# Kernel optimization log

Measured on AMD Instinct MI355X. Metric: run time of the kernel, lower is better.

Reference implementation:

```python
import jax, jax.numpy as jnp
import numpy as np

N_PROD, N_CUST = 100000, 50000
HID, OUT = 128, 64
E_PP, E_PC, E_LB = 800000, 800000, 400000


def sage(x_src, x_dst, src, dst, Wl, bl, Wr, n_dst):
    # PyG SAGEConv (mean aggr): lin_l(mean_{j->i} x_j) + lin_r(x_i); bias on lin_l only
    msg = x_src[src]                                             # [E, d] gather
    s = jax.ops.segment_sum(msg, dst, num_segments=n_dst)        # [n_dst, d]
    cnt = jax.ops.segment_sum(jnp.ones((src.shape[0],), x_src.dtype), dst, num_segments=n_dst)
    mean = s / jnp.maximum(cnt, 1.0)[:, None]
    return mean @ Wl.T + bl + x_dst @ Wr.T


def setup_inputs() -> dict:
    key = jax.random.key(0)
    ks = iter(jax.random.split(key, 40))

    def lin_w(i, o):
        return (jax.random.normal(next(ks), (o, i), jnp.float32) / np.sqrt(i))

    inp = {}
    inp['x_product'] = jax.random.normal(next(ks), (N_PROD, HID), jnp.float32)
    inp['x_customer'] = jax.random.normal(next(ks), (N_CUST, HID), jnp.float32)
    inp['ei_pp'] = jax.random.randint(next(ks), (2, E_PP), 0, N_PROD)
    src_pc = jax.random.randint(next(ks), (1, E_PC), 0, N_PROD)
    dst_pc = jax.random.randint(next(ks), (1, E_PC), 0, N_CUST)
    inp['ei_pc'] = jnp.concatenate([src_pc, dst_pc], axis=0)
    row = jax.random.randint(next(ks), (1, E_LB), 0, N_CUST)
    col = jax.random.randint(next(ks), (1, E_LB), 0, N_PROD)
    inp['edge_label_index'] = jnp.concatenate([row, col], axis=0)

    # ItemGNNEncoder params
    inp['it_W1l'], inp['it_W1r'] = lin_w(HID, HID), lin_w(HID, HID)
    inp['it_b1'] = jnp.zeros((HID,), jnp.float32)
    inp['it_W2l'], inp['it_W2r'] = lin_w(HID, HID), lin_w(HID, HID)
    inp['it_b2'] = jnp.zeros((HID,), jnp.float32)
    inp['it_Wlin'] = lin_w(HID, OUT)
    inp['it_blin'] = jnp.zeros((OUT,), jnp.float32)
    # UserGNNEncoder params
    inp['us_W1l'], inp['us_W1r'] = lin_w(HID, HID), lin_w(HID, HID)
    inp['us_b1'] = jnp.zeros((HID,), jnp.float32)
    inp['us_W2l'], inp['us_W2r'] = lin_w(HID, HID), lin_w(HID, HID)
    inp['us_b2'] = jnp.zeros((HID,), jnp.float32)
    inp['us_W3l'], inp['us_W3r'] = lin_w(HID, HID), lin_w(HID, HID)
    inp['us_b3'] = jnp.zeros((HID,), jnp.float32)
    inp['us_Wlin'] = lin_w(HID, OUT)
    inp['us_blin'] = jnp.zeros((OUT,), jnp.float32)
    # EdgeDecoder params
    inp['de_W1'] = lin_w(2 * OUT, OUT)
    inp['de_b1'] = jnp.zeros((OUT,), jnp.float32)
    inp['de_W2'] = lin_w(OUT, 1)
    inp['de_b2'] = jnp.zeros((1,), jnp.float32)
    return inp


def reference(x_product, x_customer, ei_pp, ei_pc, edge_label_index,
              it_W1l, it_b1, it_W1r, it_W2l, it_b2, it_W2r, it_Wlin, it_blin,
              us_W1l, us_b1, us_W1r, us_W2l, us_b2, us_W2r, us_W3l, us_b3, us_W3r,
              us_Wlin, us_blin, de_W1, de_b1, de_W2, de_b2):
    pp_s, pp_d = ei_pp[0], ei_pp[1]
    pc_s, pc_d = ei_pc[0], ei_pc[1]

    # ItemGNNEncoder on product-product metapath
    p = jax.nn.relu(sage(x_product, x_product, pp_s, pp_d, it_W1l, it_b1, it_W1r, N_PROD))
    p = jax.nn.relu(sage(p, p, pp_s, pp_d, it_W2l, it_b2, it_W2r, N_PROD))
    z_prod = p @ it_Wlin.T + it_blin                              # [N_PROD, OUT]

    # UserGNNEncoder
    px = jax.nn.relu(sage(x_product, x_product, pp_s, pp_d, us_W1l, us_b1, us_W1r, N_PROD))
    cx = jax.nn.relu(sage(x_product, x_customer, pc_s, pc_d, us_W2l, us_b2, us_W2r, N_CUST))
    cx = jax.nn.relu(sage(px, cx, pc_s, pc_d, us_W3l, us_b3, us_W3r, N_CUST))
    z_cust = cx @ us_Wlin.T + us_blin                             # [N_CUST, OUT]

    # EdgeDecoder: gather-concat-MLP
    row, col = edge_label_index[0], edge_label_index[1]
    z = jnp.concatenate([z_cust[row], z_prod[col]], axis=-1)      # [E_LB, 2*OUT]
    z = jax.nn.relu(z @ de_W1.T + de_b1)
    return z @ de_W2.T + de_b2                                    # [E_LB, 1]
```

## Files before the change

### kernel.cpp

```cpp
#include <hip/hip_runtime.h>
#include <hip/hip_bf16.h>

#define HID   128
#define OUTD  64
#define NPROD 100000
#define NCUST 50000
#define EPP   800000
#define EPC   800000
#define ELB   400000
#define NBK   391
#define EBLK  4096
#define RCAP3 512
#define BCAP3 2560
#define CPADN 400

typedef __bf16 bf16x8 __attribute__((ext_vector_type(8)));
typedef float  f32x4  __attribute__((ext_vector_type(4)));
typedef unsigned short u16;
typedef unsigned int u32;

__device__ __forceinline__ float b2f(u16 u) {
  unsigned int v = ((unsigned int)u) << 16;
  float f; __builtin_memcpy(&f, &v, 4); return f;
}
__device__ __forceinline__ u16 f2b(float f) {
  __hip_bfloat16 h = __float2bfloat16(f);
  u16 u; __builtin_memcpy(&u, &h, 2); return u;
}

union Pack8 { u16 u[8]; int4 v; };

__device__ __forceinline__ int sidx(int row, int chunk) {
  return row * HID + ((chunk ^ (row & 15)) << 3);
}
__device__ __forceinline__ int sidx64(int row, int chunk) {
  return row * 64 + ((chunk ^ (row & 7)) << 3);
}

__global__ __launch_bounds__(256) void k_cast(const float* __restrict__ src,
                                              u16* __restrict__ dst, int n8) {
  int i = blockIdx.x * 256 + threadIdx.x;
  if (i >= n8) return;
  float4 a = ((const float4*)src)[2 * i];
  float4 b = ((const float4*)src)[2 * i + 1];
  Pack8 p;
  p.u[0] = f2b(a.x); p.u[1] = f2b(a.y); p.u[2] = f2b(a.z); p.u[3] = f2b(a.w);
  p.u[4] = f2b(b.x); p.u[5] = f2b(b.y); p.u[6] = f2b(b.z); p.u[7] = f2b(b.w);
  ((int4*)dst)[i] = p.v;
}

#define NJOBS 13
struct CastJobs { const float* src[NJOBS]; int n8[NJOBS]; };

__global__ __launch_bounds__(256) void k_cast_w(CastJobs jobs, u16* __restrict__ wbuf) {
  int job = blockIdx.x >> 3;
  int idx = (blockIdx.x & 7) * 256 + threadIdx.x;
  int off8 = (job < 10) ? job * 2048 : 10 * 2048 + (job - 10) * 1024;
  if (idx >= jobs.n8[job]) return;
  const float* s = jobs.src[job];
  float4 a = ((const float4*)s)[2 * idx];
  float4 b = ((const float4*)s)[2 * idx + 1];
  Pack8 p;
  p.u[0] = f2b(a.x); p.u[1] = f2b(a.y); p.u[2] = f2b(a.z); p.u[3] = f2b(a.w);
  p.u[4] = f2b(b.x); p.u[5] = f2b(b.y); p.u[6] = f2b(b.z); p.u[7] = f2b(b.w);
  ((int4*)wbuf)[off8 + idx] = p.v;
}

__global__ __launch_bounds__(256) void k_bucket3(const int* __restrict__ ei_pp,
                                                 const int* __restrict__ ei_pc,
                                                 int* __restrict__ bfill_pp,
                                                 int* __restrict__ bfill_pc,
                                                 u32* __restrict__ bss_pp,
                                                 u32* __restrict__ bss_pc) {
  __shared__ int lcnt[NBK], lstart[NBK], lfill[NBK], gbase[NBK];
  __shared__ u32 spay[EBLK];
  __shared__ u16 sbk[EBLK];
  __shared__ int wtot[4];
  const int t = threadIdx.x;
  const int lane = t & 63, wv = t >> 6;
  int xcc; asm("s_getreg_b32 %0, hwreg(HW_REG_XCC_ID)" : "=s"(xcc));
  const int rep = xcc & 7;
  const int NBLK_PP = (EPP + EBLK - 1) / EBLK;
  const bool isPP = (int)blockIdx.x < NBLK_PP;
  const int* ei = isPP ? ei_pp : ei_pc;
  const int E  = isPP ? EPP : EPC;
  const int SH = isPP ? 8 : 7;
  int* bfill = isPP ? bfill_pp : bfill_pc;
  u32* bss   = isPP ? bss_pp : bss_pc;
  const int base = (isPP ? (int)blockIdx.x : (int)blockIdx.x - NBLK_PP) * EBLK;
  const int n = min(EBLK, E - base);

  for (int j = t; j < NBK; j += 256) { lcnt[j] = 0; lfill[j] = 0; }
  __syncthreads();

  u32 pay[16]; int bk[16];
  #pragma unroll
  for (int i = 0; i < 16; ++i) {
    int idx = i * 256 + t;
    bk[i] = -1;
    if (idx < n) {
      int e = base + idx;
      int s = ei[e];
      int d = ei[E + e];
      int b = d >> SH;
      bk[i] = b;
      pay[i] = ((u32)s << SH) | (u32)(d & ((1 << SH) - 1));
      atomicAdd(&lcnt[b], 1);
    }
  }
  __syncthreads();
  {
    int a0 = (2 * t < NBK) ? lcnt[2 * t] : 0;
    int a1 = (2 * t + 1 < NBK) ? lcnt[2 * t + 1] : 0;
    int s = a0 + a1;
    #pragma unroll
    for (int d = 1; d < 64; d <<= 1) {
      int u = __shfl_up(s, d, 64);
      if (lane >= d) s += u;
    }
    if (lane == 63) wtot[wv] = s;
    __syncthreads();
    int wpre = 0;
    for (int w = 0; w < wv; ++w) wpre += wtot[w];
    int excl = s + wpre - (a0 + a1);
    if (2 * t < NBK) lstart[2 * t] = excl;
    if (2 * t + 1 < NBK) lstart[2 * t + 1] = excl + a0;
  }
  __syncthreads();
  for (int b = t; b < NBK; b += 256) {
    int c = lcnt[b];
    gbase[b] = c ? atomicAdd(&bfill[(rep * CPADN + b) << 4], c) : 0;
  }
  #pragma unroll
  for (int i = 0; i < 16; ++i) {
    if (bk[i] >= 0) {
      int pos = lstart[bk[i]] + atomicAdd(&lfill[bk[i]], 1);
      spay[pos] = pay[i];
      sbk[pos] = (u16)bk[i];
    }
  }
  __syncthreads();
  for (int i = t; i < n; i += 256) {
    int b = sbk[i];
    int slot = gbase[b] + (i - lstart[b]);
    if (slot < RCAP3)
      bss[(b * 8 + rep) * RCAP3 + slot] = spay[i];
  }
}

template <int K, int SHL>
__global__ __launch_bounds__(256) void k_bsort(const u32* __restrict__ bss,
                                               const int* __restrict__ bfill,
                                               int* __restrict__ gctr,
                                               int* __restrict__ esrc,
                                               int* __restrict__ start,
                                               int* __restrict__ cnt,
                                               int n_nodes) {
  __shared__ u32 pairs[BCAP3];
  __shared__ int outsrc[BCAP3];
  __shared__ int lcnt[K], lstart[K], lfill[K];
  __shared__ int sh_n, sh_base, rn[8], roff[8];
  const int b = blockIdx.x, tid = threadIdx.x;
  if (tid < 8) rn[tid] = min(bfill[(tid * CPADN + b) << 4], RCAP3);
  for (int j = tid; j < K; j += 256) { lcnt[j] = 0; lfill[j] = 0; }
  __syncthreads();
  if (tid == 0) {
    int run = 0;
    for (int r = 0; r < 8; ++r) {
      roff[r] = run;
      int m = min(rn[r], BCAP3 - run);
      rn[r] = m;
      run += m;
    }
    sh_n = run;
    sh_base = atomicAdd(gctr, run);
  }
  __syncthreads();
  const int n = sh_n, base = sh_base;
  #pragma unroll
  for (int r = 0; r < 8; ++r) {
    int m = rn[r], o = roff[r];
    for (int i = tid; i < m; i += 256) {
      u32 p = bss[(b * 8 + r) * RCAP3 + i];
      pairs[o + i] = p;
      atomicAdd(&lcnt[p & (K - 1)], 1);
    }
  }
  __syncthreads();
  if (tid == 0) {
    int run = 0;
    for (int j = 0; j < K; ++j) { lstart[j] = run; run += lcnt[j]; }
  }
  __syncthreads();
  for (int i = tid; i < n; i += 256) {
    u32 p = pairs[i];
    int ln = p & (K - 1);
    int pos = lstart[ln] + atomicAdd(&lfill[ln], 1);
    outsrc[pos] = (int)(p >> SHL);
  }
  __syncthreads();
  for (int i = tid; i < n; i += 256) esrc[base + i] = outsrc[i];
  const int nb0 = b * K;
  for (int j = tid; j < K; j += 256) {
    int g = nb0 + j;
    if (g < n_nodes) { start[g] = base + lstart[j]; cnt[g] = lcnt[j]; }
  }
}

__global__ __launch_bounds__(256) void k_agg2(const int* __restrict__ es_a,
                                              const int* __restrict__ st_a,
                                              const int* __restrict__ cn_a,
                                              const u16* __restrict__ xa,
                                              u16* __restrict__ oa, int na,
                                              const int* __restrict__ es_b,
                                              const int* __restrict__ st_b,
                                              const int* __restrict__ cn_b,
                                              const u16* __restrict__ xb,
                                              u16* __restrict__ ob, int nb, int blkA) {
  const int t = threadIdx.x;
  const bool A = (int)blockIdx.x < blkA;
  const int node = (A ? (int)blockIdx.x : (int)blockIdx.x - blkA) * 16 + (t >> 4);
  const int l16 = t & 15;
  const int q4  = t & 48;
  if (node >= (A ? na : nb)) return;
  const int* esrc  = A ? es_a : es_b;
  const u16* x     = A ? xa : xb;
  u16* outm        = A ? oa : ob;
  int s0 = (A ? st_a : st_b)[node];
  int c  = (A ? cn_a : cn_b)[node];
  float acc[8] = {0.f, 0.f, 0.f, 0.f, 0.f, 0.f, 0.f, 0.f};
  for (int j0 = 0; j0 < c; j0 += 16) {
    int nch = min(16, c - j0);
    int eid = (l16 < nch) ? esrc[s0 + j0 + l16] : 0;
    int k = 0;
    for (; k + 4 <= nch; k += 4) {
      int s0i = __shfl(eid, q4 + k, 64);
      int s1i = __shfl(eid, q4 + k + 1, 64);
      int s2i = __shfl(eid, q4 + k + 2, 64);
      int s3i = __shfl(eid, q4 + k + 3, 64);
      Pack8 p0, p1, p2, p3;
      p0.v = *(const int4*)(x + (size_t)s0i * HID + l16 * 8);
      p1.v = *(const int4*)(x + (size_t)s1i * HID + l16 * 8);
      p2.v = *(const int4*)(x + (size_t)s2i * HID + l16 * 8);
      p3.v = *(const int4*)(x + (size_t)s3i * HID + l16 * 8);
      #pragma unroll
      for (int u = 0; u < 8; ++u)
        acc[u] += (b2f(p0.u[u]) + b2f(p1.u[u])) + (b2f(p2.u[u]) + b2f(p3.u[u]));
    }
    for (; k < nch; ++k) {
      int s = __shfl(eid, q4 + k, 64);
      Pack8 p;
      p.v = *(const int4*)(x + (size_t)s * HID + l16 * 8);
      #pragma unroll
      for (int u = 0; u < 8; ++u) acc[u] += b2f(p.u[u]);
    }
  }
  float inv = 1.0f / (float)max(c, 1);
  Pack8 o;
  #pragma unroll
  for (int u = 0; u < 8; ++u) o.u[u] = f2b(acc[u] * inv);
  *(int4*)(outm + (size_t)node * HID + l16 * 8) = o.v;
}

template <bool RELU, bool A2F, bool CHAIN, bool CHB>
__global__ __launch_bounds__(256) void k_gemm(const u16* __restrict__ A1,
                                              const u16* __restrict__ W1,
                                              const void* __restrict__ A2v,
                                              const u16* __restrict__ W2,
                                              const float* __restrict__ bias,
                                              u16* __restrict__ out, int M,
                                              const u16* __restrict__ Wlin,
                                              const float* __restrict__ blin,
                                              const u16* __restrict__ dW1,
                                              const float* __restrict__ db1) {
  __shared__ __align__(16) u16 sA[64 * HID];
  __shared__ __align__(16) u16 sW[128 * HID];
  const int tid  = threadIdx.x;
  const int lane = tid & 63;
  const int wave = tid >> 6;
  const int q    = lane >> 4;
  const int r16  = lane & 15;
  const int m0   = blockIdx.x * 64;

  f32x4 acc[4][2];
  #pragma unroll
  for (int i = 0; i < 4; ++i)
    #pragma unroll
    for (int j = 0; j < 2; ++j) {
      acc[i][j][0] = 0.f; acc[i][j][1] = 0.f; acc[i][j][2] = 0.f; acc[i][j][3] = 0.f;
    }

  #pragma unroll
  for (int phase = 0; phase < 2; ++phase) {
    const u16* W = phase ? W2 : W1;
    if (phase) __syncthreads();
    #pragma unroll
    for (int i = 0; i < 4; ++i) {
      int idx = i * 256 + tid;
      int rr = idx >> 4, c8 = idx & 15;
      int gr = m0 + rr;
      Pack8 p; p.v = make_int4(0, 0, 0, 0);
      if (gr < M) {
        if (phase == 0 || !A2F) {
          const u16* A = phase ? (const u16*)A2v : A1;
          p.v = *(const int4*)(A + (size_t)gr * HID + c8 * 8);
        } else {
          const float* A = (const float*)A2v;
          const float* s = A + (size_t)gr * HID + c8 * 8;
          float4 f0 = ((const float4*)s)[0], f1 = ((const float4*)s)[1];
          p.u[0] = f2b(f0.x); p.u[1] = f2b(f0.y); p.u[2] = f2b(f0.z); p.u[3] = f2b(f0.w);
          p.u[4] = f2b(f1.x); p.u[5] = f2b(f1.y); p.u[6] = f2b(f1.z); p.u[7] = f2b(f1.w);
        }
      }
      *(int4*)(sA + sidx(rr, c8)) = p.v;
    }
    #pragma unroll
    for (int i = 0; i < 8; ++i) {
      int idx = i * 256 + tid;
      int rr = idx >> 4, c8 = idx & 15;
      *(int4*)(sW + sidx(rr, c8)) = *(const int4*)(W + (size_t)rr * HID + c8 * 8);
    }
    __syncthreads();
    #pragma unroll
    for (int ks = 0; ks < 4; ++ks) {
      int chunk = ks * 4 + q;
      bf16x8 a[4], b[2];
      #pragma unroll
      for (int mi = 0; mi < 4; ++mi)
        a[mi] = *(const bf16x8*)(sA + sidx(mi * 16 + r16, chunk));
      #pragma unroll
      for (int ni = 0; ni < 2; ++ni)
        b[ni] = *(const bf16x8*)(sW + sidx(wave * 32 + ni * 16 + r16, chunk));
      #pragma unroll
      for (int mi = 0; mi < 4; ++mi)
        #pragma unroll
        for (int ni = 0; ni < 2; ++ni)
          acc[mi][ni] = __builtin_amdgcn_mfma_f32_16x16x32_bf16(a[mi], b[ni], acc[mi][ni], 0, 0, 0);
    }
  }

  if (!CHAIN) {
    #pragma unroll
    for (int ni = 0; ni < 2; ++ni) {
      int col = wave * 32 + ni * 16 + r16;
      float bv = bias[col];
      #pragma unroll
      for (int mi = 0; mi < 4; ++mi)
        #pragma unroll
        for (int r = 0; r < 4; ++r) {
          int gr = m0 + mi * 16 + q * 4 + r;
          if (gr < M) {
            float v = acc[mi][ni][r] + bv;
            if (RELU) v = fmaxf(v, 0.f);
            out[(size_t)gr * HID + col] = f2b(v);
          }
        }
    }
    return;
  }

  __syncthreads();
  #pragma unroll
  for (int ni = 0; ni < 2; ++ni) {
    int col = wave * 32 + ni * 16 + r16;
    float bv = bias[col];
    #pragma unroll
    for (int mi = 0; mi < 4; ++mi)
      #pragma unroll
      for (int r = 0; r < 4; ++r) {
        int rl = mi * 16 + q * 4 + r;
        float v = acc[mi][ni][r] + bv;
        if (RELU) v = fmaxf(v, 0.f);
        sA[rl * HID + (((col >> 3) ^ (rl & 15)) << 3) + (col & 7)] = f2b(v);
      }
  }
  #pragma unroll
  for (int i = 0; i < 4; ++i) {
    int idx = i * 256 + tid;
    int rr = idx >> 4, c8 = idx & 15;
    *(int4*)(sW + sidx(rr, c8)) = *(const int4*)(Wlin + (size_t)rr * HID + c8 * 8);
  }
  #pragma unroll
  for (int i = 0; i < 2; ++i) {
    int idx = i * 256 + tid;
    int rr = idx >> 3, c8 = idx & 7;
    *(int4*)(sW + 8192 + sidx64(rr, c8)) = *(const int4*)(dW1 + (size_t)rr * HID + c8 * 8);
  }
  __syncthreads();
  f32x4 az[4];
  #pragma unroll
  for (int i = 0; i < 4; ++i) { az[i][0]=0.f; az[i][1]=0.f; az[i][2]=0.f; az[i][3]=0.f; }
  #pragma unroll
  for (int ks = 0; ks < 4; ++ks) {
    int chunk = ks * 4 + q;
    bf16x8 b = *(const bf16x8*)(sW + sidx(wave * 16 + r16, chunk));
    #pragma unroll
    for (int mi = 0; mi < 4; ++mi) {
      bf16x8 a = *(const bf16x8*)(sA + sidx(mi * 16 + r16, chunk));
      az[mi] = __builtin_amdgcn_mfma_f32_16x16x32_bf16(a, b, az[mi], 0, 0, 0);
    }
  }
  {
    int col = wave * 16 + r16;
    float bl = blin[col];
    #pragma unroll
    for (int mi = 0; mi < 4; ++mi)
      #pragma unroll
      for (int r = 0; r < 4; ++r) {
        int rl = mi * 16 + q * 4 + r;
        sW[12288 + rl * 64 + (((col >> 3) ^ (rl & 7)) << 3) + (col & 7)] = f2b(az[mi][r] + bl);
      }
  }
  __syncthreads();
  f32x4 au[4];
  #pragma unroll
  for (int i = 0; i < 4; ++i) { au[i][0]=0.f; au[i][1]=0.f; au[i][2]=0.f; au[i][3]=0.f; }
  #pragma unroll
  for (int ks = 0; ks < 2; ++ks) {
    int chunk = ks * 4 + q;
    bf16x8 b = *(const bf16x8*)(sW + 8192 + sidx64(wave * 16 + r16, chunk));
    #pragma unroll
    for (int mi = 0; mi < 4; ++mi) {
      bf16x8 a = *(const bf16x8*)(sW + 12288 + sidx64(mi * 16 + r16, chunk));
      au[mi] = __builtin_amdgcn_mfma_f32_16x16x32_bf16(a, b, au[mi], 0, 0, 0);
    }
  }
  {
    int col = wave * 16 + r16;
    float db = CHB ? db1[col] : 0.f;
    #pragma unroll
    for (int mi = 0; mi < 4; ++mi)
      #pragma unroll
      for (int r = 0; r < 4; ++r) {
        int gr = m0 + mi * 16 + q * 4 + r;
        if (gr < M) out[(size_t)gr * 64 + col] = f2b(au[mi][r] + db);
      }
  }
}

__global__ __launch_bounds__(256) void k_gemm2o(const u16* __restrict__ A1,
                                                const u16* __restrict__ A2,
                                                const u16* __restrict__ Wa,
                                                const u16* __restrict__ Wb,
                                                const u16* __restrict__ Wc,
                                                const u16* __restrict__ Wd,
                                                const float* __restrict__ bias1,
                                                const float* __restrict__ bias2,
                                                u16* __restrict__ out1,
                                                u16* __restrict__ out2, int M) {
  __shared__ __align__(16) u16 sA1[64 * HID];
  __shared__ __align__(16) u16 sA2[64 * HID];
  __shared__ __align__(16) u16 sW[128 * HID];
  const int tid  = threadIdx.x;
  const int lane = tid & 63;
  const int wave = tid >> 6;
  const int q    = lane >> 4;
  const int r16  = lane & 15;
  const int m0   = blockIdx.x * 64;

  f32x4 acc1[4][2], acc2[4][2];
  #pragma unroll
  for (int i = 0; i < 4; ++i)
    #pragma unroll
    for (int j = 0; j < 2; ++j) {
      acc1[i][j][0] = 0.f; acc1[i][j][1] = 0.f; acc1[i][j][2] = 0.f; acc1[i][j][3] = 0.f;
      acc2[i][j][0] = 0.f; acc2[i][j][1] = 0.f; acc2[i][j][2] = 0.f; acc2[i][j][3] = 0.f;
    }

  #pragma unroll
  for (int i = 0; i < 4; ++i) {
    int idx = i * 256 + tid;
    int rr = idx >> 4, c8 = idx & 15;
    int gr = m0 + rr;
    Pack8 p1, p2;
    p1.v = make_int4(0, 0, 0, 0);
    p2.v = make_int4(0, 0, 0, 0);
    if (gr < M) {
      p1.v = *(const int4*)(A1 + (size_t)gr * HID + c8 * 8);
      p2.v = *(const int4*)(A2 + (size_t)gr * HID + c8 * 8);
    }
    *(int4*)(sA1 + sidx(rr, c8)) = p1.v;
    *(int4*)(sA2 + sidx(rr, c8)) = p2.v;
  }

  auto mfmaPhase = [&](const u16* sA, f32x4 (&acc)[4][2]) {
    #pragma unroll
    for (int ks = 0; ks < 4; ++ks) {
      int chunk = ks * 4 + q;
      bf16x8 a[4], b[2];
      #pragma unroll
      for (int mi = 0; mi < 4; ++mi)
        a[mi] = *(const bf16x8*)(sA + sidx(mi * 16 + r16, chunk));
      #pragma unroll
      for (int ni = 0; ni < 2; ++ni)
        b[ni] = *(const bf16x8*)(sW + sidx(wave * 32 + ni * 16 + r16, chunk));
      #pragma unroll
      for (int mi = 0; mi < 4; ++mi)
        #pragma unroll
        for (int ni = 0; ni < 2; ++ni)
          acc[mi][ni] = __builtin_amdgcn_mfma_f32_16x16x32_bf16(a[mi], b[ni], acc[mi][ni], 0, 0, 0);
    }
  };

  #pragma unroll
  for (int phase = 0; phase < 4; ++phase) {
    const u16* W = (phase == 0) ? Wa : (phase == 1) ? Wb : (phase == 2) ? Wc : Wd;
    if (phase) __syncthreads();
    #pragma unroll
    for (int i = 0; i < 8; ++i) {
      int idx = i * 256 + tid;
      int rr = idx >> 4, c8 = idx & 15;
      *(int4*)(sW + sidx(rr, c8)) = *(const int4*)(W + (size_t)rr * HID + c8 * 8);
    }
    __syncthreads();
    if (phase == 0)      mfmaPhase(sA1, acc1);
    else if (phase == 1) mfmaPhase(sA2, acc1);
    else if (phase == 2) mfmaPhase(sA1, acc2);
    else                 mfmaPhase(sA2, acc2);
  }

  #pragma unroll
  for (int ni = 0; ni < 2; ++ni) {
    int col = wave * 32 + ni * 16 + r16;
    float bv1 = bias1[col];
    float bv2 = bias2[col];
    #pragma unroll
    for (int mi = 0; mi < 4; ++mi)
      #pragma unroll
      for (int r = 0; r < 4; ++r) {
        int gr = m0 + mi * 16 + q * 4 + r;
        if (gr < M) {
          out1[(size_t)gr * HID + col] = f2b(fmaxf(acc1[mi][ni][r] + bv1, 0.f));
          out2[(size_t)gr * HID + col] = f2b(fmaxf(acc2[mi][ni][r] + bv2, 0.f));
        }
      }
  }
}

__global__ __launch_bounds__(256) void k_edge(const u16* __restrict__ U,
                                              const u16* __restrict__ V,
                                              const int* __restrict__ eli,
                                              const float* __restrict__ w2,
                                              const float* __restrict__ b2,
                                              float* __restrict__ out) {
  const int lane = threadIdx.x & 63;
  const int wave = threadIdx.x >> 6;
  const int se   = (lane >> 3);
  const int ch   = lane & 7;
  float w2c[8];
  #pragma unroll
  for (int j = 0; j < 8; ++j) w2c[j] = w2[ch * 8 + j];
  const float b2v = b2[0];
  const int e0 = blockIdx.x * 256;
  #pragma unroll
  for (int p = 0; p < 8; ++p) {
    int e = e0 + p * 32 + wave * 8 + se;
    if (e < ELB) {
      int r = eli[e];
      int c = eli[ELB + e];
      Pack8 pu, pv;
      pu.v = *(const int4*)(U + (size_t)r * 64 + ch * 8);
      pv.v = *(const int4*)(V + (size_t)c * 64 + ch * 8);
      float s = 0.f;
      #pragma unroll
      for (int j = 0; j < 8; ++j)
        s += fmaxf(b2f(pu.u[j]) + b2f(pv.u[j]), 0.f) * w2c[j];
      s += __shfl_xor(s, 1, 64);
      s += __shfl_xor(s, 2, 64);
      s += __shfl_xor(s, 4, 64);
      if (ch == 0) out[e] = s + b2v;
    }
  }
}

extern "C" void kernel_launch(void* const* d_in, const int* in_sizes, int n_in,
                              void* d_out, int out_size, void* d_ws, size_t ws_size,
                              hipStream_t stream) {
  const float* x_prod = (const float*)d_in[0];
  const float* x_cust = (const float*)d_in[1];
  const int* ei_pp    = (const int*)d_in[2];
  const int* ei_pc    = (const int*)d_in[3];
  const int* eli      = (const int*)d_in[4];

  const float *it_W1l, *it_W1r, *it_b1, *it_W2l, *it_W2r, *it_b2, *it_Wlin, *it_blin;
  const float *us_W1l, *us_W1r, *us_b1, *us_W2l, *us_W2r, *us_b2;
  const float *us_W3l, *us_W3r, *us_b3, *us_Wlin, *us_blin;
  if (in_sizes[6] == 128) {
    it_W1l  = (const float*)d_in[5];  it_b1   = (const float*)d_in[6];  it_W1r  = (const float*)d_in[7];
    it_W2l  = (const float*)d_in[8];  it_b2   = (const float*)d_in[9];  it_W2r  = (const float*)d_in[10];
    it_Wlin = (const float*)d_in[11]; it_blin = (const float*)d_in[12];
    us_W1l  = (const float*)d_in[13]; us_b1   = (const float*)d_in[14]; us_W1r  = (const float*)d_in[15];
    us_W2l  = (const float*)d_in[16]; us_b2   = (const float*)d_in[17]; us_W2r  = (const float*)d_in[18];
    us_W3l  = (const float*)d_in[19]; us_b3   = (const float*)d_in[20]; us_W3r  = (const float*)d_in[21];
    us_Wlin = (const float*)d_in[22]; us_blin = (const float*)d_in[23];
  } else {
    it_W1l  = (const float*)d_in[5];  it_W1r  = (const float*)d_in[6];  it_b1   = (const float*)d_in[7];
    it_W2l  = (const float*)d_in[8];  it_W2r  = (const float*)d_in[9];  it_b2   = (const float*)d_in[10];
    it_Wlin = (const float*)d_in[11]; it_blin = (const float*)d_in[12];
    us_W1l  = (const float*)d_in[13]; us_W1r  = (const float*)d_in[14]; us_b1   = (const float*)d_in[15];
    us_W2l  = (const float*)d_in[16]; us_W2r  = (const float*)d_in[17]; us_b2   = (const float*)d_in[18];
    us_W3l  = (const float*)d_in[19]; us_W3r  = (const float*)d_in[20]; us_b3   = (const float*)d_in[21];
    us_Wlin = (const float*)d_in[22]; us_blin = (const float*)d_in[23];
  }
  const float* de_W1 = (const float*)d_in[24];
  const float* de_b1 = (const float*)d_in[25];
  const float* de_W2 = (const float*)d_in[26];
  const float* de_b2 = (const float*)d_in[27];

  char* ws = (char*)d_ws;
  int* bfill_pp = (int*)(ws + 0);
  int* bfill_pc = (int*)(ws + 409600);
  int* gctr     = (int*)(ws + 819200);
  int* start_pp = (int*)(ws + 819264);
  int* cnt_pp   = (int*)(ws + 1219264);
  int* start_pc = (int*)(ws + 1619264);
  int* cnt_pc   = (int*)(ws + 1819264);
  int* esrc_pp  = (int*)(ws + 2019264);
  int* esrc_pc  = (int*)(ws + 5219264);
  u16* wbuf  = (u16*)(ws + 8419264);
  u16* XPB   = (u16*)(ws + 8796096);
  u16* meanb = (u16*)(ws + 34396096);
  u16* P1    = (u16*)(ws + 59996096);
  u16* meanc = (u16*)(ws + 85596096);
  u16* CX    = (u16*)(ws + 98396096);
  u32* bss_pp = (u32*)P1;
  u32* bss_pc = (u32*)(ws + 59996096 + 6553600);
  u16* PX = XPB;
  u16* U  = (u16*)esrc_pp;
  u16* V  = CX;

  u16* w_it1l = wbuf + 0 * 16384;  u16* w_it1r = wbuf + 1 * 16384;
  u16* w_it2l = wbuf + 2 * 16384;  u16* w_it2r = wbuf + 3 * 16384;
  u16* w_us1l = wbuf + 4 * 16384;  u16* w_us1r = wbuf + 5 * 16384;
  u16* w_us2l = wbuf + 6 * 16384;  u16* w_us2r = wbuf + 7 * 16384;
  u16* w_us3l = wbuf + 8 * 16384;  u16* w_us3r = wbuf + 9 * 16384;
  u16* w_itlin = wbuf + 10 * 16384;
  u16* w_uslin = wbuf + 10 * 16384 + 8192;
  u16* w_deW1  = wbuf + 10 * 16384 + 2 * 8192;

  (void)n_in; (void)out_size; (void)ws_size;

  hipMemsetAsync(d_ws, 0, 819208, stream);

  dim3 B(256);
  k_cast<<<dim3((NPROD * HID / 8 + 255) / 256), B, 0, stream>>>(x_prod, XPB, NPROD * HID / 8);
  CastJobs jobs;
  jobs.src[0] = it_W1l;  jobs.src[1] = it_W1r;  jobs.src[2] = it_W2l;  jobs.src[3] = it_W2r;
  jobs.src[4] = us_W1l;  jobs.src[5] = us_W1r;  jobs.src[6] = us_W2l;  jobs.src[7] = us_W2r;
  jobs.src[8] = us_W3l;  jobs.src[9] = us_W3r;
  jobs.src[10] = it_Wlin; jobs.src[11] = us_Wlin; jobs.src[12] = de_W1;
  for (int i = 0; i < 10; ++i) jobs.n8[i] = 2048;
  for (int i = 10; i < 13; ++i) jobs.n8[i] = 1024;
  k_cast_w<<<dim3(NJOBS * 8), B, 0, stream>>>(jobs, wbuf);

  const int NBLK_PP = (EPP + EBLK - 1) / EBLK;
  const int NBLK_PC = (EPC + EBLK - 1) / EBLK;
  k_bucket3<<<dim3(NBLK_PP + NBLK_PC), B, 0, stream>>>(ei_pp, ei_pc, bfill_pp, bfill_pc,
                                                       bss_pp, bss_pc);
  k_bsort<256, 8><<<dim3(NBK), B, 0, stream>>>(bss_pp, bfill_pp, gctr, esrc_pp, start_pp, cnt_pp, NPROD);
  k_bsort<128, 7><<<dim3(NBK), B, 0, stream>>>(bss_pc, bfill_pc, gctr + 1, esrc_pc, start_pc, cnt_pc, NCUST);

  dim3 Gp((NPROD + 63) / 64), Gc((NCUST + 63) / 64);
  const int App = (NPROD + 15) / 16, Apc = (NCUST + 15) / 16;

  k_agg2<<<dim3(App + Apc), B, 0, stream>>>(esrc_pp, start_pp, cnt_pp, XPB, meanb, NPROD,
                                            esrc_pc, start_pc, cnt_pc, XPB, meanc, NCUST, App);
  k_gemm<true, true, false, false><<<Gc, B, 0, stream>>>(
      meanc, w_us2l, x_cust, w_us2r, us_b2, CX, NCUST, nullptr, nullptr, nullptr, nullptr);
  k_gemm2o<<<Gp, B, 0, stream>>>(meanb, XPB, w_it1l, w_it1r, w_us1l, w_us1r,
                                 it_b1, us_b1, P1, PX, NPROD);
  k_agg2<<<dim3(App + Apc), B, 0, stream>>>(esrc_pp, start_pp, cnt_pp, P1, meanb, NPROD,
                                            esrc_pc, start_pc, cnt_pc, PX, meanc, NCUST, App);
  k_gemm<true, false, true, true><<<Gc, B, 0, stream>>>(
      meanc, w_us3l, CX, w_us3r, us_b3, U, NCUST, w_uslin, us_blin, w_deW1, de_b1);
  k_gemm<true, false, true, false><<<Gp, B, 0, stream>>>(
      meanb, w_it2l, P1, w_it2r, it_b2, V, NPROD, w_itlin, it_blin, w_deW1 + 64, nullptr);
  k_edge<<<dim3((ELB + 255) / 256), B, 0, stream>>>(U, V, eli, de_W2, de_b2, (float*)d_out);
}
```

Measured before the change: 513.4 us.

## Merge prep, bucket-sort and chained GEMM launches into fewer fused kernels

Folds the input cast, the weight cast and the edge bucketing into one k_prep launch. The two per-graph bucket sorts become one k_bsort2 launch, and its serial single-thread prefix sum is replaced by a wave-shuffle parallel scan. The two chained GEMM tail kernels become one k_chain2 launch covering both customer and product tiles. The aim is to cut launch count and inter-kernel gaps and let independent small kernels share the GPU; the cost is branchy mixed-role kernels whose shared-memory footprint applies to the cast blocks too, which may reduce occupancy there.

Measured after the change: 489.0 us. -4.7%, faster.

```diff
diff --git a/kernel.cpp b/kernel.cpp
--- a/kernel.cpp
+++ b/kernel.cpp
@@ -13,6 +13,8 @@
 #define RCAP3 512
 #define BCAP3 2560
 #define CPADN 400
+#define NB3   392
+#define NCAST 6250
 
 typedef __bf16 bf16x8 __attribute__((ext_vector_type(8)));
 typedef float  f32x4  __attribute__((ext_vector_type(4)));
@@ -37,57 +39,64 @@
   return row * 64 + ((chunk ^ (row & 7)) << 3);
 }
 
-__global__ __launch_bounds__(256) void k_cast(const float* __restrict__ src,
-                                              u16* __restrict__ dst, int n8) {
-  int i = blockIdx.x * 256 + threadIdx.x;
-  if (i >= n8) return;
-  float4 a = ((const float4*)src)[2 * i];
-  float4 b = ((const float4*)src)[2 * i + 1];
-  Pack8 p;
-  p.u[0] = f2b(a.x); p.u[1] = f2b(a.y); p.u[2] = f2b(a.z); p.u[3] = f2b(a.w);
-  p.u[4] = f2b(b.x); p.u[5] = f2b(b.y); p.u[6] = f2b(b.z); p.u[7] = f2b(b.w);
-  ((int4*)dst)[i] = p.v;
-}
-
 #define NJOBS 13
 struct CastJobs { const float* src[NJOBS]; int n8[NJOBS]; };
 
-__global__ __launch_bounds__(256) void k_cast_w(CastJobs jobs, u16* __restrict__ wbuf) {
-  int job = blockIdx.x >> 3;
-  int idx = (blockIdx.x & 7) * 256 + threadIdx.x;
-  int off8 = (job < 10) ? job * 2048 : 10 * 2048 + (job - 10) * 1024;
-  if (idx >= jobs.n8[job]) return;
-  const float* s = jobs.src[job];
-  float4 a = ((const float4*)s)[2 * idx];
-  float4 b = ((const float4*)s)[2 * idx + 1];
-  Pack8 p;
-  p.u[0] = f2b(a.x); p.u[1] = f2b(a.y); p.u[2] = f2b(a.z); p.u[3] = f2b(a.w);
-  p.u[4] = f2b(b.x); p.u[5] = f2b(b.y); p.u[6] = f2b(b.z); p.u[7] = f2b(b.w);
-  ((int4*)wbuf)[off8 + idx] = p.v;
-}
-
-__global__ __launch_bounds__(256) void k_bucket3(const int* __restrict__ ei_pp,
-                                                 const int* __restrict__ ei_pc,
-                                                 int* __restrict__ bfill_pp,
-                                                 int* __restrict__ bfill_pc,
-                                                 u32* __restrict__ bss_pp,
-                                                 u32* __restrict__ bss_pc) {
+__global__ __launch_bounds__(256) void k_prep(const int* __restrict__ ei_pp,
+                                              const int* __restrict__ ei_pc,
+                                              int* __restrict__ bfill_pp,
+                                              int* __restrict__ bfill_pc,
+                                              u32* __restrict__ bss_pp,
+                                              u32* __restrict__ bss_pc,
+                                              const float* __restrict__ x_prod,
+                                              u16* __restrict__ XPB,
+                                              CastJobs jobs,
+                                              u16* __restrict__ wbuf) {
   __shared__ int lcnt[NBK], lstart[NBK], lfill[NBK], gbase[NBK];
   __shared__ u32 spay[EBLK];
   __shared__ u16 sbk[EBLK];
   __shared__ int wtot[4];
   const int t = threadIdx.x;
+  int bid = blockIdx.x;
+
+  if (bid >= NB3) {
+    bid -= NB3;
+    if (bid < NCAST) {
+      int i = bid * 256 + t;
+      float4 a = ((const float4*)x_prod)[2 * i];
+      float4 b = ((const float4*)x_prod)[2 * i + 1];
+      Pack8 p;
+      p.u[0] = f2b(a.x); p.u[1] = f2b(a.y); p.u[2] = f2b(a.z); p.u[3] = f2b(a.w);
+      p.u[4] = f2b(b.x); p.u[5] = f2b(b.y); p.u[6] = f2b(b.z); p.u[7] = f2b(b.w);
+      ((int4*)XPB)[i] = p.v;
+      return;
+    }
+    bid -= NCAST;
+    int job = bid >> 3;
+    int idx = (bid & 7) * 256 + t;
+    int off8 = (job < 10) ? job * 2048 : 10 * 2048 + (job - 10) * 1024;
+    if (idx >= jobs.n8[job]) return;
+    const float* s = jobs.src[job];
+    float4 a = ((const float4*)s)[2 * idx];
+    float4 b = ((const float4*)s)[2 * idx + 1];
+    Pack8 p;
+    p.u[0] = f2b(a.x); p.u[1] = f2b(a.y); p.u[2] = f2b(a.z); p.u[3] = f2b(a.w);
+    p.u[4] = f2b(b.x); p.u[5] = f2b(b.y); p.u[6] = f2b(b.z); p.u[7] = f2b(b.w);
+    ((int4*)wbuf)[off8 + idx] = p.v;
+    return;
+  }
+
   const int lane = t & 63, wv = t >> 6;
   int xcc; asm("s_getreg_b32 %0, hwreg(HW_REG_XCC_ID)" : "=s"(xcc));
   const int rep = xcc & 7;
   const int NBLK_PP = (EPP + EBLK - 1) / EBLK;
-  const bool isPP = (int)blockIdx.x < NBLK_PP;
+  const bool isPP = bid < NBLK_PP;
   const int* ei = isPP ? ei_pp : ei_pc;
   const int E  = isPP ? EPP : EPC;
   const int SH = isPP ? 8 : 7;
   int* bfill = isPP ? bfill_pp : bfill_pc;
   u32* bss   = isPP ? bss_pp : bss_pc;
-  const int base = (isPP ? (int)blockIdx.x : (int)blockIdx.x - NBLK_PP) * EBLK;
+  const int base = (isPP ? bid : bid - NBLK_PP) * EBLK;
   const int n = min(EBLK, E - base);
 
   for (int j = t; j < NBK; j += 256) { lcnt[j] = 0; lfill[j] = 0; }
@@ -148,19 +157,35 @@
   }
 }
 
-template <int K, int SHL>
-__global__ __launch_bounds__(256) void k_bsort(const u32* __restrict__ bss,
-                                               const int* __restrict__ bfill,
-                                               int* __restrict__ gctr,
-                                               int* __restrict__ esrc,
-                                               int* __restrict__ start,
-                                               int* __restrict__ cnt,
-                                               int n_nodes) {
+__global__ __launch_bounds__(256) void k_bsort2(const u32* __restrict__ bss_pp,
+                                                const int* __restrict__ bfill_pp,
+                                                const u32* __restrict__ bss_pc,
+                                                const int* __restrict__ bfill_pc,
+                                                int* __restrict__ gctr,
+                                                int* __restrict__ esrc_pp,
+                                                int* __restrict__ start_pp,
+                                                int* __restrict__ cnt_pp,
+                                                int* __restrict__ esrc_pc,
+                                                int* __restrict__ start_pc,
+                                                int* __restrict__ cnt_pc) {
   __shared__ u32 pairs[BCAP3];
   __shared__ int outsrc[BCAP3];
-  __shared__ int lcnt[K], lstart[K], lfill[K];
-  __shared__ int sh_n, sh_base, rn[8], roff[8];
-  const int b = blockIdx.x, tid = threadIdx.x;
+  __shared__ int lcnt[256], lstart[256], lfill[256];
+  __shared__ int sh_n, sh_base, rn[8], roff[8], wtot[4];
+  const int tid = threadIdx.x;
+  const int lane = tid & 63, wv = tid >> 6;
+  const bool isPP = (int)blockIdx.x < NBK;
+  const int b = isPP ? (int)blockIdx.x : (int)blockIdx.x - NBK;
+  const int K   = isPP ? 256 : 128;
+  const int SHL = isPP ? 8 : 7;
+  const u32* bss   = isPP ? bss_pp : bss_pc;
+  const int* bfill = isPP ? bfill_pp : bfill_pc;
+  int* gc    = isPP ? gctr : gctr + 1;
+  int* esrc  = isPP ? esrc_pp : esrc_pc;
+  int* start = isPP ? start_pp : start_pc;
+  int* cnt   = isPP ? cnt_pp : cnt_pc;
+  const int n_nodes = isPP ? NPROD : NCUST;
+
   if (tid < 8) rn[tid] = min(bfill[(tid * CPADN + b) << 4], RCAP3);
   for (int j = tid; j < K; j += 256) { lcnt[j] = 0; lfill[j] = 0; }
   __syncthreads();
@@ -173,28 +198,42 @@
       run += m;
     }
     sh_n = run;
-    sh_base = atomicAdd(gctr, run);
+    sh_base = atomicAdd(gc, run);
   }
   __syncthreads();
   const int n = sh_n, base = sh_base;
+  const int Km1 = K - 1;
   #pragma unroll
   for (int r = 0; r < 8; ++r) {
     int m = rn[r], o = roff[r];
     for (int i = tid; i < m; i += 256) {
       u32 p = bss[(b * 8 + r) * RCAP3 + i];
       pairs[o + i] = p;
-      atomicAdd(&lcnt[p & (K - 1)], 1);
-    }
-  }
-  __syncthreads();
-  if (tid == 0) {
-    int run = 0;
-    for (int j = 0; j < K; ++j) { lstart[j] = run; run += lcnt[j]; }
+      atomicAdd(&lcnt[p & Km1], 1);
+    }
+  }
+  __syncthreads();
+  {
+    int a0 = (2 * tid < K) ? lcnt[2 * tid] : 0;
+    int a1 = (2 * tid + 1 < K) ? lcnt[2 * tid + 1] : 0;
+    int s = a0 + a1;
+    #pragma unroll
+    for (int d = 1; d < 64; d <<= 1) {
+      int u = __shfl_up(s, d, 64);
+      if (lane >= d) s += u;
+    }
+    if (lane == 63) wtot[wv] = s;
+    __syncthreads();
+    int wpre = 0;
+    for (int w = 0; w < wv; ++w) wpre += wtot[w];
+    int excl = s + wpre - (a0 + a1);
+    if (2 * tid < K) lstart[2 * tid] = excl;
+    if (2 * tid + 1 < K) lstart[2 * tid + 1] = excl + a0;
   }
   __syncthreads();
   for (int i = tid; i < n; i += 256) {
     u32 p = pairs[i];
-    int ln = p & (K - 1);
+    int ln = p & Km1;
     int pos = lstart[ln] + atomicAdd(&lfill[ln], 1);
     outsrc[pos] = (int)(p >> SHL);
   }
@@ -262,17 +301,13 @@
   *(int4*)(outm + (size_t)node * HID + l16 * 8) = o.v;
 }
 
-template <bool RELU, bool A2F, bool CHAIN, bool CHB>
+template <bool RELU, bool A2F>
 __global__ __launch_bounds__(256) void k_gemm(const u16* __restrict__ A1,
                                               const u16* __restrict__ W1,
                                               const void* __restrict__ A2v,
                                               const u16* __restrict__ W2,
                                               const float* __restrict__ bias,
-                                              u16* __restrict__ out, int M,
-                                              const u16* __restrict__ Wlin,
-                                              const float* __restrict__ blin,
-                                              const u16* __restrict__ dW1,
-                                              const float* __restrict__ db1) {
+                                              u16* __restrict__ out, int M) {
   __shared__ __align__(16) u16 sA[64 * HID];
   __shared__ __align__(16) u16 sW[128 * HID];
   const int tid  = threadIdx.x;
@@ -339,27 +374,6 @@
     }
   }
 
-  if (!CHAIN) {
-    #pragma unroll
-    for (int ni = 0; ni < 2; ++ni) {
-      int col = wave * 32 + ni * 16 + r16;
-      float bv = bias[col];
-      #pragma unroll
-      for (int mi = 0; mi < 4; ++mi)
-        #pragma unroll
-        for (int r = 0; r < 4; ++r) {
-          int gr = m0 + mi * 16 + q * 4 + r;
-          if (gr < M) {
-            float v = acc[mi][ni][r] + bv;
-            if (RELU) v = fmaxf(v, 0.f);
-            out[(size_t)gr * HID + col] = f2b(v);
-          }
-        }
-    }
-    return;
-  }
-
-  __syncthreads();
   #pragma unroll
   for (int ni = 0; ni < 2; ++ni) {
     int col = wave * 32 + ni * 16 + r16;
@@ -368,9 +382,108 @@
     for (int mi = 0; mi < 4; ++mi)
       #pragma unroll
       for (int r = 0; r < 4; ++r) {
+        int gr = m0 + mi * 16 + q * 4 + r;
+        if (gr < M) {
+          float v = acc[mi][ni][r] + bv;
+          if (RELU) v = fmaxf(v, 0.f);
+          out[(size_t)gr * HID + col] = f2b(v);
+        }
+      }
+  }
+}
+
+__global__ __launch_bounds__(256) void k_chain2(
+    const u16* __restrict__ A1a, const u16* __restrict__ W1a,
+    const u16* __restrict__ A2a, const u16* __restrict__ W2a,
+    const float* __restrict__ biasa, u16* __restrict__ outa, int Ma,
+    const u16* __restrict__ Wlina, const float* __restrict__ blina,
+    const u16* __restrict__ dW1a, const float* __restrict__ db1a,
+    const u16* __restrict__ A1b, const u16* __restrict__ W1b,
+    const u16* __restrict__ A2b, const u16* __restrict__ W2b,
+    const float* __restrict__ biasb, u16* __restrict__ outb, int Mb,
+    const u16* __restrict__ Wlinb, const float* __restrict__ blinb,
+    const u16* __restrict__ dW1b, const float* __restrict__ db1b,
+    int blkA) {
+  __shared__ __align__(16) u16 sA[64 * HID];
+  __shared__ __align__(16) u16 sW[128 * HID];
+  const bool isA = (int)blockIdx.x < blkA;
+  const u16* A1 = isA ? A1a : A1b;
+  const u16* W1 = isA ? W1a : W1b;
+  const u16* A2 = isA ? A2a : A2b;
+  const u16* W2 = isA ? W2a : W2b;
+  const float* bias = isA ? biasa : biasb;
+  u16* out = isA ? outa : outb;
+  const int M = isA ? Ma : Mb;
+  const u16* Wlin = isA ? Wlina : Wlinb;
+  const float* blin = isA ? blina : blinb;
+  const u16* dW1 = isA ? dW1a : dW1b;
+  const float* db1 = isA ? db1a : db1b;
+
+  const int tid  = threadIdx.x;
+  const int lane = tid & 63;
+  const int wave = tid >> 6;
+  const int q    = lane >> 4;
+  const int r16  = lane & 15;
+  const int m0   = (isA ? (int)blockIdx.x : (int)blockIdx.x - blkA) * 64;
+
+  f32x4 acc[4][2];
+  #pragma unroll
+  for (int i = 0; i < 4; ++i)
+    #pragma unroll
+    for (int j = 0; j < 2; ++j) {
+      acc[i][j][0] = 0.f; acc[i][j][1] = 0.f; acc[i][j][2] = 0.f; acc[i][j][3] = 0.f;
+    }
+
+  #pragma unroll
+  for (int phase = 0; phase < 2; ++phase) {
+    const u16* W = phase ? W2 : W1;
+    const u16* A = phase ? A2 : A1;
+    if (phase) __syncthreads();
+    #pragma unroll
+    for (int i = 0; i < 4; ++i) {
+      int idx = i * 256 + tid;
+      int rr = idx >> 4, c8 = idx & 15;
+      int gr = m0 + rr;
+      Pack8 p; p.v = make_int4(0, 0, 0, 0);
+      if (gr < M) p.v = *(const int4*)(A + (size_t)gr * HID + c8 * 8);
+      *(int4*)(sA + sidx(rr, c8)) = p.v;
+    }
+    #pragma unroll
+    for (int i = 0; i < 8; ++i) {
+      int idx = i * 256 + tid;
+      int rr = idx >> 4, c8 = idx & 15;
+      *(int4*)(sW + sidx(rr, c8)) = *(const int4*)(W + (size_t)rr * HID + c8 * 8);
+    }
+    __syncthreads();
+    #pragma unroll
+    for (int ks = 0; ks < 4; ++ks) {
+      int chunk = ks * 4 + q;
+      bf16x8 a[4], b[2];
+      #pragma unroll
+      for (int mi = 0; mi < 4; ++mi)
+        a[mi] = *(const bf16x8*)(sA + sidx(mi * 16 + r16, chunk));
+      #pragma unroll
+      for (int ni = 0; ni < 2; ++ni)
+        b[ni] = *(const bf16x8*)(sW + sidx(wave * 32 + ni * 16 + r16, chunk));
+      #pragma unroll
+      for (int mi = 0; mi < 4; ++mi)
+        #pragma unroll
+        for (int ni = 0; ni < 2; ++ni)
+          acc[mi][ni] = __builtin_amdgcn_mfma_f32_16x16x32_bf16(a[mi], b[ni], acc[mi][ni], 0, 0, 0);
+    }
+  }
+
+  __syncthreads();
+  #pragma unroll
+  for (int ni = 0; ni < 2; ++ni) {
+    int col = wave * 32 + ni * 16 + r16;
+    float bv = bias[col];
+    #pragma unroll
+    for (int mi = 0; mi < 4; ++mi)
+      #pragma unroll
+      for (int r = 0; r < 4; ++r) {
         int rl = mi * 16 + q * 4 + r;
-        float v = acc[mi][ni][r] + bv;
-        if (RELU) v = fmaxf(v, 0.f);
+        float v = fmaxf(acc[mi][ni][r] + bv, 0.f);
         sA[rl * HID + (((col >> 3) ^ (rl & 15)) << 3) + (col & 7)] = f2b(v);
       }
   }
@@ -427,7 +540,7 @@
   }
   {
     int col = wave * 16 + r16;
-    float db = CHB ? db1[col] : 0.f;
+    float db = db1 ? db1[col] : 0.f;
     #pragma unroll
     for (int mi = 0; mi < 4; ++mi)
       #pragma unroll
@@ -643,7 +756,6 @@
   hipMemsetAsync(d_ws, 0, 819208, stream);
 
   dim3 B(256);
-  k_cast<<<dim3((NPROD * HID / 8 + 255) / 256), B, 0, stream>>>(x_prod, XPB, NPROD * HID / 8);
   CastJobs jobs;
   jobs.src[0] = it_W1l;  jobs.src[1] = it_W1r;  jobs.src[2] = it_W2l;  jobs.src[3] = it_W2r;
   jobs.src[4] = us_W1l;  jobs.src[5] = us_W1r;  jobs.src[6] = us_W2l;  jobs.src[7] = us_W2r;
@@ -651,29 +763,27 @@
   jobs.src[10] = it_Wlin; jobs.src[11] = us_Wlin; jobs.src[12] = de_W1;
   for (int i = 0; i < 10; ++i) jobs.n8[i] = 2048;
   for (int i = 10; i < 13; ++i) jobs.n8[i] = 1024;
-  k_cast_w<<<dim3(NJOBS * 8), B, 0, stream>>>(jobs, wbuf);
-
-  const int NBLK_PP = (EPP + EBLK - 1) / EBLK;
-  const int NBLK_PC = (EPC + EBLK - 1) / EBLK;
-  k_bucket3<<<dim3(NBLK_PP + NBLK_PC), B, 0, stream>>>(ei_pp, ei_pc, bfill_pp, bfill_pc,
-                                                       bss_pp, bss_pc);
-  k_bsort<256, 8><<<dim3(NBK), B, 0, stream>>>(bss_pp, bfill_pp, gctr, esrc_pp, start_pp, cnt_pp, NPROD);
-  k_bsort<128, 7><<<dim3(NBK), B, 0, stream>>>(bss_pc, bfill_pc, gctr + 1, esrc_pc, start_pc, cnt_pc, NCUST);
+
+  k_prep<<<dim3(NB3 + NCAST + NJOBS * 8), B, 0, stream>>>(
+      ei_pp, ei_pc, bfill_pp, bfill_pc, bss_pp, bss_pc, x_prod, XPB, jobs, wbuf);
+  k_bsort2<<<dim3(2 * NBK), B, 0, stream>>>(bss_pp, bfill_pp, bss_pc, bfill_pc, gctr,
+                                            esrc_pp, start_pp, cnt_pp,
+                                            esrc_pc, start_pc, cnt_pc);
 
   dim3 Gp((NPROD + 63) / 64), Gc((NCUST + 63) / 64);
   const int App = (NPROD + 15) / 16, Apc = (NCUST + 15) / 16;
 
   k_agg2<<<dim3(App + Apc), B, 0, stream>>>(esrc_pp, start_pp, cnt_pp, XPB, meanb, NPROD,
                                             esrc_pc, start_pc, cnt_pc, XPB, meanc, NCUST, App);
-  k_gemm<true, true, false, false><<<Gc, B, 0, stream>>>(
-      meanc, w_us2l, x_cust, w_us2r, us_b2, CX, NCUST, nullptr, nullptr, nullptr, nullptr);
+  k_gemm<true, true><<<Gc, B, 0, stream>>>(
+      meanc, w_us2l, x_cust, w_us2r, us_b2, CX, NCUST);
   k_gemm2o<<<Gp, B, 0, stream>>>(meanb, XPB, w_it1l, w_it1r, w_us1l, w_us1r,
                                  it_b1, us_b1, P1, PX, NPROD);
   k_agg2<<<dim3(App + Apc), B, 0, stream>>>(esrc_pp, start_pp, cnt_pp, P1, meanb, NPROD,
                                             esrc_pc, start_pc, cnt_pc, PX, meanc, NCUST, App);
-  k_gemm<true, false, true, true><<<Gc, B, 0, stream>>>(
-      meanc, w_us3l, CX, w_us3r, us_b3, U, NCUST, w_uslin, us_blin, w_deW1, de_b1);
-  k_gemm<true, false, true, false><<<Gp, B, 0, stream>>>(
-      meanb, w_it2l, P1, w_it2r, it_b2, V, NPROD, w_itlin, it_blin, w_deW1 + 64, nullptr);
+  k_chain2<<<dim3(782 + 1563), B, 0, stream>>>(
+      meanc, w_us3l, CX, w_us3r, us_b3, U, NCUST, w_uslin, us_blin, w_deW1, de_b1,
+      meanb, w_it2l, P1, w_it2r, it_b2, V, NPROD, w_itlin, it_blin, w_deW1 + 64, nullptr,
+      782);
   k_edge<<<dim3((ELB + 255) / 256), B, 0, stream>>>(U, V, eli, de_W2, de_b2, (float*)d_out);
 }
```
